# Kernel tuning notes

Measured on AMD Instinct MI355X. Metric: run time of the kernel, lower is better.

## Reference

```python
import jax, jax.numpy as jnp
import numpy as np

B, L, E, H = 4, 2048, 1024, 16
D = E // H  # per-head dim

def setup_inputs() -> dict:
    key = jax.random.key(0)
    ks = jax.random.split(key, 12)
    xav = lambda k, shape: jax.random.normal(k, shape, jnp.float32) * (2.0 / (shape[0] + shape[-1])) ** 0.5
    embeddings = jax.random.normal(ks[0], (B, L, E), jnp.float32)
    pre_proj_w = xav(ks[1], (E, E)); pre_proj_b = jnp.zeros((E,), jnp.float32)
    pre_sparse_w = xav(ks[2], (E, E)); pre_sparse_b = jnp.zeros((E,), jnp.float32)
    toeplitz_psfs = xav(ks[3], (H, 2 * L - 1, D))
    post_conv_w = xav(ks[4], (E, E)); post_conv_b = jnp.zeros((E,), jnp.float32)
    dens = 0.01
    num_nz = int(L * L * dens)
    idxs = jax.random.randint(ks[5], (num_nz, 2), 0, L)
    vals = jnp.abs(jax.random.normal(ks[6], (num_nz,), jnp.float32))
    sparse = jnp.zeros((L, L), jnp.float32).at[idxs[:, 0], idxs[:, 1]].add(vals)
    ln_gamma = jnp.ones((E,), jnp.float32); ln_beta = jnp.zeros((E,), jnp.float32)
    return {"embeddings": embeddings, "pre_proj_w": pre_proj_w, "pre_proj_b": pre_proj_b,
            "pre_sparse_w": pre_sparse_w, "pre_sparse_b": pre_sparse_b,
            "toeplitz_psfs": toeplitz_psfs, "post_conv_w": post_conv_w, "post_conv_b": post_conv_b,
            "sparse": sparse, "ln_gamma": ln_gamma, "ln_beta": ln_beta}

def reference(embeddings, pre_proj_w, pre_proj_b, pre_sparse_w, pre_sparse_b,
              toeplitz_psfs, post_conv_w, post_conv_b, sparse, ln_gamma, ln_beta):
    b, l, e = embeddings.shape
    h, two_l_m1, d = toeplitz_psfs.shape
    # causal PSF mask: first l taps kept, trailing l-1 zeroed (before softmax)
    psf_mask = jnp.concatenate([jnp.ones((l,)), jnp.zeros((l - 1,))])[None, :, None]
    psfs = jax.nn.softmax(toeplitz_psfs * psf_mask, axis=1)  # softmax over 2l-1 taps
    # pre-projection
    pre = jnp.einsum('ble,oe->blo', embeddings, pre_proj_w) + pre_proj_b
    # pad seq to 2l-1 and split heads: [b, h, 2l-1, d]
    padded = jnp.pad(pre, ((0, 0), (0, l - 1), (0, 0)))
    padded = padded.reshape(b, two_l_m1, h, d).transpose(0, 2, 1, 3)
    # 2D FFT convolution over (seq, per-head-dim)
    psf_fft = jnp.fft.fftn(psfs, axes=(1, 2))              # [h, 2l-1, d]
    emb_fft = jnp.fft.fftn(padded, axes=(2, 3))            # [b, h, 2l-1, d]
    conv = jnp.real(jnp.fft.ifftn(psf_fft[None] * emb_fft, axes=(2, 3)))[:, :, :l, :]
    conv = jax.nn.gelu(conv, approximate=False)
    conv = conv.transpose(0, 2, 1, 3).reshape(b, l, e)
    conv_emb = jnp.einsum('ble,oe->blo', conv, post_conv_w) + post_conv_b
    # sparse branch (causal lower-triangular mask)
    sparse_masked = sparse * jnp.tril(jnp.ones((l, l), sparse.dtype))
    pre_sparse = jnp.einsum('ble,oe->blo', pre, pre_sparse_w) + pre_sparse_b
    sparse_emb = jnp.einsum('ls,bse->ble', sparse_masked, pre_sparse)
    # residual + layernorm (dropout = identity at eval)
    x = conv_emb + sparse_emb + embeddings
    mu = jnp.mean(x, axis=-1, keepdims=True)
    var = jnp.mean(jnp.square(x - mu), axis=-1, keepdims=True)
    return (x - mu) * jax.lax.rsqrt(var + 1e-12) * ln_gamma + ln_beta
```

## Files before the change

kernel.cpp:

```cpp
#include <hip/hip_runtime.h>
#include <hip/hip_bf16.h>
#include <hip/hip_fp16.h>
#include <math.h>

#define B_ 4
#define L_ 2048
#define E_ 1024
#define H_ 16
#define D_ 64
#define NFFT 4096
#define CAP 128

typedef __hip_bfloat16 bf16;
typedef __attribute__((ext_vector_type(8))) short bf16x8;
typedef __attribute__((ext_vector_type(4))) float f32x4;
typedef __attribute__((ext_vector_type(2))) __fp16 f16x2;

typedef __attribute__((address_space(1))) const unsigned int gas_u32;
typedef __attribute__((address_space(3))) unsigned int las_u32;

__device__ __forceinline__ void gload_lds16(const void* g, void* l) {
    __builtin_amdgcn_global_load_lds((gas_u32*)g, (las_u32*)l, 16, 0, 0);
}

#define SL(i) ((i) + ((i) >> 4))
#define LDSN (NFFT + NFFT / 16)
#define FST 65

__device__ __forceinline__ float bfu2f(unsigned short u) {
    return __uint_as_float(((unsigned)u) << 16);
}
__device__ __forceinline__ f16x2 pk2(float a, float b) {
    return __builtin_amdgcn_cvt_pkrtz(a, b);
}

__device__ __forceinline__ int drev64(int k) {
    return ((k & 3) << 4) | (k & 12) | ((k >> 4) & 3);
}

#define C1R 0.923879532511287f
#define C1I -0.382683432365090f
#define C2R 0.707106781186548f
#define C2I -0.707106781186548f
#define C3R 0.382683432365090f
#define C3I -0.923879532511287f

__device__ __forceinline__ void r4dif_w(float& x0r, float& x0i, float& x1r, float& x1i,
                                        float& x2r, float& x2i, float& x3r, float& x3i,
                                        float w1r, float w1i) {
    float a0r = x0r + x2r, a0i = x0i + x2i, a1r = x0r - x2r, a1i = x0i - x2i;
    float a2r = x1r + x3r, a2i = x1i + x3i, a3r = x1r - x3r, a3i = x1i - x3i;
    float y0r = a0r + a2r, y0i = a0i + a2i, y2r = a0r - a2r, y2i = a0i - a2i;
    float y1r = a1r + a3i, y1i = a1i - a3r, y3r = a1r - a3i, y3i = a1i + a3r;
    float w2r = w1r * w1r - w1i * w1i, w2i = 2.0f * w1r * w1i;
    float w3r = w2r * w1r - w2i * w1i, w3i = w2r * w1i + w2i * w1r;
    x0r = y0r; x0i = y0i;
    x1r = y1r * w1r - y1i * w1i; x1i = y1r * w1i + y1i * w1r;
    x2r = y2r * w2r - y2i * w2i; x2i = y2r * w2i + y2i * w2r;
    x3r = y3r * w3r - y3i * w3i; x3i = y3r * w3i + y3i * w3r;
}
__device__ __forceinline__ void r4dif_nt(float& x0r, float& x0i, float& x1r, float& x1i,
                                         float& x2r, float& x2i, float& x3r, float& x3i) {
    float a0r = x0r + x2r, a0i = x0i + x2i, a1r = x0r - x2r, a1i = x0i - x2i;
    float a2r = x1r + x3r, a2i = x1i + x3i, a3r = x1r - x3r, a3i = x1i - x3i;
    x0r = a0r + a2r; x0i = a0i + a2i;
    x2r = a0r - a2r; x2i = a0i - a2i;
    float y1r = a1r + a3i, y1i = a1i - a3r, y3r = a1r - a3i, y3i = a1i + a3r;
    x1r = y1r; x1i = y1i; x3r = y3r; x3i = y3i;
}
__device__ __forceinline__ void r4dit_w(float& x0r, float& x0i, float& x1r, float& x1i,
                                        float& x2r, float& x2i, float& x3r, float& x3i,
                                        float w1r, float w1i) {
    float w2r = w1r * w1r - w1i * w1i, w2i = 2.0f * w1r * w1i;
    float w3r = w2r * w1r - w2i * w1i, w3i = w2r * w1i + w2i * w1r;
    float z1r = x1r * w1r + x1i * w1i, z1i = x1i * w1r - x1r * w1i;
    float z2r = x2r * w2r + x2i * w2i, z2i = x2i * w2r - x2r * w2i;
    float z3r = x3r * w3r + x3i * w3i, z3i = x3i * w3r - x3r * w3i;
    float b0r = x0r + z2r, b0i = x0i + z2i, b1r = x0r - z2r, b1i = x0i - z2i;
    float b2r = z1r + z3r, b2i = z1i + z3i, b3r = z1r - z3r, b3i = z1i - z3i;
    x0r = b0r + b2r; x0i = b0i + b2i;
    x2r = b0r - b2r; x2i = b0i - b2i;
    x1r = b1r - b3i; x1i = b1i + b3r;
    x3r = b1r + b3i; x3i = b1i - b3r;
}
__device__ __forceinline__ void r4dit_nt(float& x0r, float& x0i, float& x1r, float& x1i,
                                         float& x2r, float& x2i, float& x3r, float& x3i) {
    float b0r = x0r + x2r, b0i = x0i + x2i, b1r = x0r - x2r, b1i = x0i - x2i;
    float b2r = x1r + x3r, b2i = x1i + x3i, b3r = x1r - x3r, b3i = x1i - x3i;
    x0r = b0r + b2r; x0i = b0i + b2i;
    x2r = b0r - b2r; x2i = b0i - b2i;
    x1r = b1r - b3i; x1i = b1i + b3r;
    x3r = b1r + b3i; x3i = b1i - b3r;
}

__device__ __forceinline__ void fftA_fwd(float* xr, float* xi, float wpr, float wpi) {
    r4dif_w(xr[0], xi[0], xr[4], xi[4], xr[8], xi[8], xr[12], xi[12], wpr, wpi);
    r4dif_w(xr[1], xi[1], xr[5], xi[5], xr[9], xi[9], xr[13], xi[13],
            wpr * C1R - wpi * C1I, wpr * C1I + wpi * C1R);
    r4dif_w(xr[2], xi[2], xr[6], xi[6], xr[10], xi[10], xr[14], xi[14],
            wpr * C2R - wpi * C2I, wpr * C2I + wpi * C2R);
    r4dif_w(xr[3], xi[3], xr[7], xi[7], xr[11], xi[11], xr[15], xi[15],
            wpr * C3R - wpi * C3I, wpr * C3I + wpi * C3R);
    float s2r = wpr * wpr - wpi * wpi, s2i = 2.0f * wpr * wpi;
    float w4r = s2r * s2r - s2i * s2i, w4i = 2.0f * s2r * s2i;
#pragma unroll
    for (int g = 0; g < 4; ++g)
        r4dif_w(xr[4 * g], xi[4 * g], xr[4 * g + 1], xi[4 * g + 1], xr[4 * g + 2],
                xi[4 * g + 2], xr[4 * g + 3], xi[4 * g + 3], w4r, w4i);
}
__device__ __forceinline__ void fftA_inv(float* xr, float* xi, float wpr, float wpi) {
    float s2r = wpr * wpr - wpi * wpi, s2i = 2.0f * wpr * wpi;
    float w4r = s2r * s2r - s2i * s2i, w4i = 2.0f * s2r * s2i;
#pragma unroll
    for (int g = 0; g < 4; ++g)
        r4dit_w(xr[4 * g], xi[4 * g], xr[4 * g + 1], xi[4 * g + 1], xr[4 * g + 2],
                xi[4 * g + 2], xr[4 * g + 3], xi[4 * g + 3], w4r, w4i);
    r4dit_w(xr[0], xi[0], xr[4], xi[4], xr[8], xi[8], xr[12], xi[12], wpr, wpi);
    r4dit_w(xr[1], xi[1], xr[5], xi[5], xr[9], xi[9], xr[13], xi[13],
            wpr * C1R - wpi * C1I, wpr * C1I + wpi * C1R);
    r4dit_w(xr[2], xi[2], xr[6], xi[6], xr[10], xi[10], xr[14], xi[14],
            wpr * C2R - wpi * C2I, wpr * C2I + wpi * C2R);
    r4dit_w(xr[3], xi[3], xr[7], xi[7], xr[11], xi[11], xr[15], xi[15],
            wpr * C3R - wpi * C3I, wpr * C3I + wpi * C3R);
}
__device__ __forceinline__ void fftB_fwd(float* xr, float* xi, float wor, float woi) {
    r4dif_w(xr[0], xi[0], xr[4], xi[4], xr[8], xi[8], xr[12], xi[12], wor, woi);
    r4dif_w(xr[1], xi[1], xr[5], xi[5], xr[9], xi[9], xr[13], xi[13],
            wor * C1R - woi * C1I, wor * C1I + woi * C1R);
    r4dif_w(xr[2], xi[2], xr[6], xi[6], xr[10], xi[10], xr[14], xi[14],
            wor * C2R - woi * C2I, wor * C2I + woi * C2R);
    r4dif_w(xr[3], xi[3], xr[7], xi[7], xr[11], xi[11], xr[15], xi[15],
            wor * C3R - woi * C3I, wor * C3I + woi * C3R);
    float s2r = wor * wor - woi * woi, s2i = 2.0f * wor * woi;
    float w4r = s2r * s2r - s2i * s2i, w4i = 2.0f * s2r * s2i;
#pragma unroll
    for (int g = 0; g < 4; ++g)
        r4dif_w(xr[4 * g], xi[4 * g], xr[4 * g + 1], xi[4 * g + 1], xr[4 * g + 2],
                xi[4 * g + 2], xr[4 * g + 3], xi[4 * g + 3], w4r, w4i);
}
__device__ __forceinline__ void fftB_inv(float* xr, float* xi, float wor, float woi) {
    float s2r = wor * wor - woi * woi, s2i = 2.0f * wor * woi;
    float w4r = s2r * s2r - s2i * s2i, w4i = 2.0f * s2r * s2i;
#pragma unroll
    for (int g = 0; g < 4; ++g)
        r4dit_w(xr[4 * g], xi[4 * g], xr[4 * g + 1], xi[4 * g + 1], xr[4 * g + 2],
                xi[4 * g + 2], xr[4 * g + 3], xi[4 * g + 3], w4r, w4i);
    r4dit_w(xr[0], xi[0], xr[4], xi[4], xr[8], xi[8], xr[12], xi[12], wor, woi);
    r4dit_w(xr[1], xi[1], xr[5], xi[5], xr[9], xi[9], xr[13], xi[13],
            wor * C1R - woi * C1I, wor * C1I + woi * C1R);
    r4dit_w(xr[2], xi[2], xr[6], xi[6], xr[10], xi[10], xr[14], xi[14],
            wor * C2R - woi * C2I, wor * C2I + woi * C2R);
    r4dit_w(xr[3], xi[3], xr[7], xi[7], xr[11], xi[11], xr[15], xi[15],
            wor * C3R - woi * C3I, wor * C3I + woi * C3R);
}
__device__ __forceinline__ void fftC_fwd(float* xr, float* xi) {
    r4dif_w(xr[0], xi[0], xr[4], xi[4], xr[8], xi[8], xr[12], xi[12], 1.0f, 0.0f);
    r4dif_w(xr[1], xi[1], xr[5], xi[5], xr[9], xi[9], xr[13], xi[13], C1R, C1I);
    r4dif_w(xr[2], xi[2], xr[6], xi[6], xr[10], xi[10], xr[14], xi[14], C2R, C2I);
    r4dif_w(xr[3], xi[3], xr[7], xi[7], xr[11], xi[11], xr[15], xi[15], C3R, C3I);
#pragma unroll
    for (int g = 0; g < 4; ++g)
        r4dif_nt(xr[4 * g], xi[4 * g], xr[4 * g + 1], xi[4 * g + 1], xr[4 * g + 2],
                 xi[4 * g + 2], xr[4 * g + 3], xi[4 * g + 3]);
}
__device__ __forceinline__ void fftC_inv(float* xr, float* xi) {
#pragma unroll
    for (int g = 0; g < 4; ++g)
        r4dit_nt(xr[4 * g], xi[4 * g], xr[4 * g + 1], xi[4 * g + 1], xr[4 * g + 2],
                 xi[4 * g + 2], xr[4 * g + 3], xi[4 * g + 3]);
    r4dit_w(xr[0], xi[0], xr[4], xi[4], xr[8], xi[8], xr[12], xi[12], 1.0f, 0.0f);
    r4dit_w(xr[1], xi[1], xr[5], xi[5], xr[9], xi[9], xr[13], xi[13], C1R, C1I);
    r4dit_w(xr[2], xi[2], xr[6], xi[6], xr[10], xi[10], xr[14], xi[14], C2R, C2I);
    r4dit_w(xr[3], xi[3], xr[7], xi[7], xr[11], xi[11], xr[15], xi[15], C3R, C3I);
}

template <int CONJ, int STRIDE>
__device__ inline void fft64h(f16x2* __restrict__ X, int tid,
                              const float2* __restrict__ tw) {
    for (int st = 0; st < 3; ++st) {
        int q = 1 << (4 - 2 * st);
        __syncthreads();
        for (int it = 0; it < 4; ++it) {
            int w = tid + (it << 8);
            int lc = w & 63, bc = w >> 6;
            int p = bc & (q - 1);
            int basev = ((bc & ~(q - 1)) << 2) | p;
            int i0 = basev * STRIDE + lc, i1 = i0 + q * STRIDE,
                i2 = i1 + q * STRIDE, i3 = i2 + q * STRIDE;
            f16x2 h0 = X[i0], h1 = X[i1], h2 = X[i2], h3 = X[i3];
            float x0r = (float)h0.x, x0i = (float)h0.y;
            float x1r = (float)h1.x, x1i = (float)h1.y;
            float x2r = (float)h2.x, x2i = (float)h2.y;
            float x3r = (float)h3.x, x3i = (float)h3.y;
            float a0r = x0r + x2r, a0i = x0i + x2i;
            float a1r = x0r - x2r, a1i = x0i - x2i;
            float a2r = x1r + x3r, a2i = x1i + x3i;
            float a3r = x1r - x3r, a3i = x1i - x3i;
            float y0r = a0r + a2r, y0i = a0i + a2i;
            float y2r = a0r - a2r, y2i = a0i - a2i;
            float y1r, y1i, y3r, y3i;
            if (!CONJ) {
                y1r = a1r + a3i; y1i = a1i - a3r;
                y3r = a1r - a3i; y3i = a1i + a3r;
            } else {
                y1r = a1r - a3i; y1i = a1i + a3r;
                y3r = a1r + a3i; y3i = a1i - a3r;
            }
            int e = (p << (2 * st)) * 64;
            float2 w1 = tw[e];
            float w1x = w1.x, w1y = CONJ ? -w1.y : w1.y;
            float w2x = w1x * w1x - w1y * w1y, w2y = 2.0f * w1x * w1y;
            float w3x = w2x * w1x - w2y * w1y, w3y = w2x * w1y + w2y * w1x;
            X[i0] = pk2(y0r, y0i);
            X[i1] = pk2(y1r * w1x - y1i * w1y, y1r * w1y + y1i * w1x);
            X[i2] = pk2(y2r * w2x - y2i * w2y, y2r * w2y + y2i * w2x);
            X[i3] = pk2(y3r * w3x - y3i * w3y, y3r * w3y + y3i * w3x);
        }
    }
    __syncthreads();
}

#define NB_TW 16
#define NB_CVT 8192
#define NB_CVTW 3072
#define NB_TF 512
#define NB_SP 2048
__global__ __launch_bounds__(256) void k_prologue(const float* __restrict__ emb,
                                                  const float* __restrict__ W1,
                                                  const float* __restrict__ W2,
                                                  const float* __restrict__ W3,
                                                  const float* __restrict__ psfs,
                                                  const float* __restrict__ Sp,
                                                  float2* __restrict__ tw,
                                                  bf16* __restrict__ embb,
                                                  bf16* __restrict__ Wb,
                                                  float* __restrict__ psfT,
                                                  int* __restrict__ nnz,
                                                  int* __restrict__ idxs,
                                                  float* __restrict__ vals) {
    __shared__ float tile[64][65];
    __shared__ int cnt;
    int tid = threadIdx.x;
    int blk = blockIdx.x;
    if (blk < NB_TW) {
        int k = blk * 256 + tid;
        float ang = -(float)k * (float)(M_PI / 2048.0);
        tw[k] = make_float2(cosf(ang), sinf(ang));
        return;
    }
    blk -= NB_TW;
    if (blk < NB_CVT) {
        int i = (blk * 256 + tid) * 4;
        float4 v = *(const float4*)(emb + i);
        bf16 tmp[4];
        tmp[0] = __float2bfloat16(v.x); tmp[1] = __float2bfloat16(v.y);
        tmp[2] = __float2bfloat16(v.z); tmp[3] = __float2bfloat16(v.w);
        *(ushort4*)(embb + i) = *(ushort4*)tmp;
        return;
    }
    blk -= NB_CVT;
    if (blk < NB_CVTW) {
        int w = blk >> 10;
        const float* src = (w == 0) ? W1 : (w == 1) ? W2 : W3;
        int i = ((blk & 1023) * 256 + tid) * 4;
        float4 v = *(const float4*)(src + i);
        bf16 tmp[4];
        tmp[0] = __float2bfloat16(v.x); tmp[1] = __float2bfloat16(v.y);
        tmp[2] = __float2bfloat16(v.z); tmp[3] = __float2bfloat16(v.w);
        *(ushort4*)(Wb + (size_t)w * E_ * E_ + i) = *(ushort4*)tmp;
        return;
    }
    blk -= NB_CVTW;
    if (blk < NB_TF) {
        int z = blk >> 5;
        int r0 = (blk & 31) * 64;
        const float* in = psfs + (size_t)z * (2 * L_ - 1) * D_;
        float* out = psfT + (size_t)z * D_ * L_;
        int tx4 = (tid & 15) * 4, ty = tid >> 4;
#pragma unroll
        for (int k = 0; k < 4; ++k) {
            int r = ty + 16 * k;
            float4 v = *(const float4*)&in[(size_t)(r0 + r) * D_ + tx4];
            tile[r][tx4 + 0] = v.x; tile[r][tx4 + 1] = v.y;
            tile[r][tx4 + 2] = v.z; tile[r][tx4 + 3] = v.w;
        }
        __syncthreads();
#pragma unroll
        for (int k = 0; k < 4; ++k) {
            int c = ty + 16 * k;
            float4 w;
            w.x = tile[tx4 + 0][c]; w.y = tile[tx4 + 1][c];
            w.z = tile[tx4 + 2][c]; w.w = tile[tx4 + 3][c];
            *(float4*)&out[(size_t)c * L_ + r0 + tx4] = w;
        }
        return;
    }
    blk -= NB_TF;
    {
        int l = blk;
        if (tid == 0) cnt = 0;
        __syncthreads();
        const float* row = Sp + (size_t)l * L_;
        for (int s = tid; s <= l; s += 256) {
            float v = row[s];
            if (v != 0.0f) {
                int slot = atomicAdd(&cnt, 1);
                if (slot < CAP) { idxs[l * CAP + slot] = s; vals[l * CAP + slot] = v; }
            }
        }
        __syncthreads();
        if (tid == 0) nnz[l] = min(cnt, CAP);
    }
}

__device__ __forceinline__ void gemm_body(void* smemraw, int flat, int nwgx,
                                          const bf16* __restrict__ A,
                                          const bf16* __restrict__ Wt,
                                          const float* __restrict__ bias,
                                          bf16* __restrict__ Cb,
                                          int nwg, int N, int K) {
    bf16* As = (bf16*)smemraw;
    bf16* Bs = As + 64 * 64;
    int tid = threadIdx.x;
    int lane = tid & 63, w = tid >> 6;
    int wr = w >> 1, wc = w & 1;

    int cpx = nwg >> 3;
    int swz = (flat & 7) * cpx + (flat >> 3);
    int bx = (swz % nwgx) * 128;
    int by = (swz / nwgx) * 64;

    f32x4 zz = {0.0f, 0.0f, 0.0f, 0.0f};
    f32x4 acc[2][4];
#pragma unroll
    for (int m = 0; m < 2; ++m)
#pragma unroll
        for (int n = 0; n < 4; ++n) acc[m][n] = zz;

    int koff = (lane >> 4) * 8;
    int rsub = lane & 15;

    for (int k0 = 0; k0 < K; k0 += 64) {
#pragma unroll
        for (int i = 0; i < 2; ++i) {
            int c = tid + i * 256;
            int row = c >> 3;
            int kb = (c & 7) * 8;
            int kbs = kb ^ ((row & 7) << 3);
            gload_lds16(A + (size_t)(by + row) * K + k0 + kbs, &As[c * 8]);
        }
#pragma unroll
        for (int i = 0; i < 4; ++i) {
            int c = tid + i * 256;
            int row = c >> 3;
            int kb = (c & 7) * 8;
            int kbs = kb ^ ((row & 7) << 3);
            gload_lds16(Wt + (size_t)(bx + row) * K + k0 + kbs, &Bs[c * 8]);
        }
        __syncthreads();
#pragma unroll
        for (int half = 0; half < 2; ++half) {
            int ko = koff + half * 32;
            bf16x8 af[2], bfv[4];
#pragma unroll
            for (int m = 0; m < 2; ++m) {
                int R = wr * 32 + m * 16 + rsub;
                af[m] = *(const bf16x8*)&As[R * 64 + (ko ^ ((R & 7) << 3))];
            }
#pragma unroll
            for (int n = 0; n < 4; ++n) {
                int R = wc * 64 + n * 16 + rsub;
                bfv[n] = *(const bf16x8*)&Bs[R * 64 + (ko ^ ((R & 7) << 3))];
            }
#pragma unroll
            for (int m = 0; m < 2; ++m)
#pragma unroll
                for (int n = 0; n < 4; ++n)
                    acc[m][n] = __builtin_amdgcn_mfma_f32_16x16x32_bf16(af[m], bfv[n], acc[m][n], 0, 0, 0);
        }
        __syncthreads();
    }

    int cq = (lane >> 4) * 4;
    int cr = lane & 15;
#pragma unroll
    for (int m = 0; m < 2; ++m) {
        int row0 = by + wr * 32 + m * 16 + cq;
#pragma unroll
        for (int n = 0; n < 4; ++n) {
            int col = bx + wc * 64 + n * 16 + cr;
            float bv = bias[col];
#pragma unroll
            for (int j = 0; j < 4; ++j) {
                float v = acc[m][n][j] + bv;
                Cb[(size_t)(row0 + j) * N + col] = __float2bfloat16(v);
            }
        }
    }
}

__device__ __forceinline__ void khat_body(void* smemraw, int blk,
                                          const float* __restrict__ psfT,
                                          f16x2* __restrict__ Khat,
                                          const float2* __restrict__ tw) {
    f16x2* fl = (f16x2*)smemraw;
    float* red = (float*)(fl + LDSN);
    int u = blk & 63, h = blk >> 6;
    int tid = threadIdx.x;
    const float* col = psfT + ((size_t)(h * D_ + u)) * L_;
    int p = tid;

    float2 twp = tw[p];
    float2 two = tw[(tid & 15) * 16];

    float v[8];
#pragma unroll
    for (int j = 0; j < 8; ++j) v[j] = col[p + 256 * j];

    float lm = v[0];
#pragma unroll
    for (int j = 1; j < 8; ++j) lm = fmaxf(lm, v[j]);
    red[tid] = lm; __syncthreads();
    for (int off = 128; off > 0; off >>= 1) {
        if (tid < off) red[tid] = fmaxf(red[tid], red[tid + off]);
        __syncthreads();
    }
    float M = fmaxf(red[0], 0.0f);
    __syncthreads();

    float e[8];
    float ls = 0.0f;
#pragma unroll
    for (int j = 0; j < 8; ++j) { e[j] = expf(v[j] - M); ls += e[j]; }
    red[tid] = ls; __syncthreads();
    for (int off = 128; off > 0; off >>= 1) {
        if (tid < off) red[tid] += red[tid + off];
        __syncthreads();
    }
    float Z = red[0] + (float)(L_ - 1) * expf(-M);
    float invZ = 1.0f / Z;
    float cval = expf(-M) * invZ;

    float xr[16], xi[16];
#pragma unroll
    for (int j = 0; j < 16; ++j) {
        int i = p + 256 * j;
        xr[j] = (j < 8) ? e[j] * invZ : ((i == 2048) ? 0.0f : cval);
        xi[j] = 0.0f;
    }
    __syncthreads();

    fftA_fwd(xr, xi, twp.x, twp.y);
#pragma unroll
    for (int j = 0; j < 16; ++j) fl[SL(p + 256 * j)] = pk2(xr[j], xi[j]);
    __syncthreads();
    {
        int bb = tid >> 4, o = tid & 15;
#pragma unroll
        for (int j = 0; j < 16; ++j) {
            f16x2 hh = fl[SL(bb * 256 + o + 16 * j)];
            xr[j] = (float)hh.x; xi[j] = (float)hh.y;
        }
        fftB_fwd(xr, xi, two.x, two.y);
#pragma unroll
        for (int j = 0; j < 16; ++j)
            fl[SL(bb * 256 + o + 16 * j)] = pk2(xr[j], xi[j]);
    }
    __syncthreads();
#pragma unroll
    for (int j = 0; j < 16; ++j) {
        f16x2 hh = fl[SL(16 * tid + j)];
        xr[j] = (float)hh.x; xi[j] = (float)hh.y;
    }
    fftC_fwd(xr, xi);

    float sc = 1.0f / (float)NFFT;
    f16x2* outp = Khat + ((size_t)h * D_ + u) * NFFT + 16 * tid;
#pragma unroll
    for (int j = 0; j < 16; ++j) outp[j] = pk2(xr[j] * sc, xi[j] * sc);
}

__device__ __forceinline__ void dfft_body(void* smemraw, int blk,
                                          f16x2* __restrict__ Khat,
                                          const float2* __restrict__ tw) {
    f16x2* X = (f16x2*)smemraw;
    int tid = threadIdx.x;
    int f0 = (blk & 63) * 64, h = blk >> 6;
    f16x2* kb = Khat + (size_t)h * D_ * NFFT;
    for (int i = tid; i < 4096; i += 256) {
        int uu = i >> 6, fc = i & 63;
        X[i] = kb[(size_t)uu * NFFT + f0 + fc];
    }
    fft64h<0, 64>(X, tid, tw);
    float sc = 1.0f / 64.0f;
    for (int i = tid; i < 4096; i += 256) {
        int s = i >> 6, fc = i & 63;
        f16x2 v = X[i];
        kb[(size_t)drev64(s) * NFFT + f0 + fc] = pk2((float)v.x * sc, (float)v.y * sc);
    }
}

__device__ __forceinline__ void vfft_body(void* smemraw, int blk,
                                          const bf16* __restrict__ preb,
                                          f16x2* __restrict__ Xv,
                                          const float2* __restrict__ tw) {
    f16x2* X = (f16x2*)smemraw;
    int tid = threadIdx.x;
    int l0 = (blk & 31) * 64, h = (blk >> 5) & 15, b = blk >> 9;
    const bf16* src = preb + ((size_t)(b * L_ + l0)) * E_ + h * 64;
#pragma unroll
    for (int it = 0; it < 2; ++it) {
        int c = tid + it * 256;
        int lc = c >> 3, v8 = (c & 7) * 8;
        bf16x8 xv8 = *(const bf16x8*)(src + (size_t)lc * E_ + v8);
#pragma unroll
        for (int j = 0; j < 8; ++j)
            X[(v8 + j) * FST + lc] = pk2(bfu2f((unsigned short)xv8[j]), 0.0f);
    }
    fft64h<0, FST>(X, tid, tw);
    for (int i = tid; i < 33 * 64; i += 256) {
        int k = i >> 6, lc = i & 63;
        Xv[((size_t)(b * H_ + h) * 33 + k) * L_ + l0 + lc] = X[drev64(k) * FST + lc];
    }
}

__global__ __launch_bounds__(256) void k_gemm1_khat(const bf16* __restrict__ A,
                                                    const bf16* __restrict__ Wt,
                                                    const float* __restrict__ bias,
                                                    bf16* __restrict__ Cb,
                                                    const float* __restrict__ psfT,
                                                    f16x2* __restrict__ Khat,
                                                    const float2* __restrict__ tw) {
    __shared__ __align__(16) char smem[24576];
    int blk = blockIdx.x;
    if (blk < 1024)
        gemm_body(smem, blk, 8, A, Wt, bias, Cb, 1024, E_, E_);
    else
        khat_body(smem, blk - 1024, psfT, Khat, tw);
}

__global__ __launch_bounds__(256) void k_gemm2_dfft_vfft(const bf16* __restrict__ A,
                                                         const bf16* __restrict__ Wt,
                                                         const float* __restrict__ bias,
                                                         bf16* __restrict__ Cb,
                                                         f16x2* __restrict__ Khat,
                                                         f16x2* __restrict__ Xv,
                                                         const float2* __restrict__ tw) {
    __shared__ __align__(16) char smem[24576];
    int blk = blockIdx.x;
    if (blk < 1024)
        gemm_body(smem, blk, 8, A, Wt, bias, Cb, 1024, E_, E_);
    else if (blk < 2048)
        dfft_body(smem, blk - 1024, Khat, tw);
    else
        vfft_body(smem, blk - 2048, A, Xv, tw);
}

__global__ __launch_bounds__(256) void k_gemm3(const bf16* __restrict__ A,
                                               const bf16* __restrict__ Wt,
                                               const float* __restrict__ bias,
                                               bf16* __restrict__ Cb) {
    __shared__ __align__(16) char smem[24576];
    gemm_body(smem, blockIdx.x, 8, A, Wt, bias, Cb, 1024, E_, E_);
}

__global__ __launch_bounds__(256) void k_seqconv(f16x2* __restrict__ Xv,
                                                 const f16x2* __restrict__ Khat,
                                                 const float2* __restrict__ tw) {
    __shared__ f16x2 fl[LDSN];
    int k = blockIdx.x, h = blockIdx.y, b = blockIdx.z;
    int tid = threadIdx.x, p = tid;
    f16x2* col = Xv + ((size_t)(b * H_ + h) * 33 + k) * L_;

    float2 twp = tw[p];
    float2 two = tw[(tid & 15) * 16];

    float xr[16], xi[16];
#pragma unroll
    for (int j = 0; j < 16; ++j) {
        if (j < 8) {
            f16x2 z = col[p + 256 * j];
            xr[j] = (float)z.x; xi[j] = (float)z.y;
        } else { xr[j] = 0.0f; xi[j] = 0.0f; }
    }
    fftA_fwd(xr, xi, twp.x, twp.y);
#pragma unroll
    for (int j = 0; j < 16; ++j) fl[SL(p + 256 * j)] = pk2(xr[j], xi[j]);
    __syncthreads();
    {
        int bb = tid >> 4, o = tid & 15;
#pragma unroll
        for (int j = 0; j < 16; ++j) {
            f16x2 hh = fl[SL(bb * 256 + o + 16 * j)];
            xr[j] = (float)hh.x; xi[j] = (float)hh.y;
        }
        fftB_fwd(xr, xi, two.x, two.y);
#pragma unroll
        for (int j = 0; j < 16; ++j)
            fl[SL(bb * 256 + o + 16 * j)] = pk2(xr[j], xi[j]);
    }
    __syncthreads();
    {
        const f16x2* khp = Khat + ((size_t)h * 64 + k) * NFFT + 16 * tid;
        f16x2 kk[16];
#pragma unroll
        for (int j = 0; j < 16; ++j) kk[j] = khp[j];
#pragma unroll
        for (int j = 0; j < 16; ++j) {
            f16x2 hh = fl[SL(16 * tid + j)];
            xr[j] = (float)hh.x; xi[j] = (float)hh.y;
        }
        fftC_fwd(xr, xi);
#pragma unroll
        for (int j = 0; j < 16; ++j) {
            float kr = (float)kk[j].x, ki = (float)kk[j].y;
            float ar = xr[j], ai = xi[j];
            xr[j] = ar * kr - ai * ki;
            xi[j] = ar * ki + ai * kr;
        }
        fftC_inv(xr, xi);
#pragma unroll
        for (int j = 0; j < 16; ++j) fl[SL(16 * tid + j)] = pk2(xr[j], xi[j]);
    }
    __syncthreads();
    {
        int bb = tid >> 4, o = tid & 15;
#pragma unroll
        for (int j = 0; j < 16; ++j) {
            f16x2 hh = fl[SL(bb * 256 + o + 16 * j)];
            xr[j] = (float)hh.x; xi[j] = (float)hh.y;
        }
        fftB_inv(xr, xi, two.x, two.y);
#pragma unroll
        for (int j = 0; j < 16; ++j)
            fl[SL(bb * 256 + o + 16 * j)] = pk2(xr[j], xi[j]);
    }
    __syncthreads();
#pragma unroll
    for (int j = 0; j < 16; ++j) {
        f16x2 hh = fl[SL(p + 256 * j)];
        xr[j] = (float)hh.x; xi[j] = (float)hh.y;
    }
    fftA_inv(xr, xi, twp.x, twp.y);
#pragma unroll
    for (int j = 0; j < 8; ++j)
        col[p + 256 * j] = pk2(xr[j], xi[j]);
}

__global__ __launch_bounds__(256) void k_vifft(const f16x2* __restrict__ Xv,
                                               bf16* __restrict__ actb,
                                               const float2* __restrict__ tw) {
    __shared__ f16x2 X[64 * FST];
    int l0 = blockIdx.x * 64, h = blockIdx.y, b = blockIdx.z;
    int tid = threadIdx.x;
    for (int i = tid; i < 33 * 64; i += 256) {
        int k = i >> 6, lc = i & 63;
        X[k * FST + lc] = Xv[((size_t)(b * H_ + h) * 33 + k) * L_ + l0 + lc];
    }
    __syncthreads();
    for (int i = tid; i < 31 * 64; i += 256) {
        int k = 33 + (i >> 6), lc = i & 63;
        f16x2 z = X[(64 - k) * FST + lc];
        X[k * FST + lc] = pk2((float)z.x, -(float)z.y);
    }
    fft64h<1, FST>(X, tid, tw);
    bf16* dst = actb + ((size_t)(b * L_ + l0)) * E_ + h * 64;
#pragma unroll
    for (int it = 0; it < 2; ++it) {
        int c = tid + it * 256;
        int lc = c >> 3, m8 = (c & 7) * 8;
        unsigned short o[8];
#pragma unroll
        for (int j = 0; j < 8; ++j) {
            float x = (float)X[drev64(m8 + j) * FST + lc].x;
            float g = 0.5f * x * (1.0f + erff(x * 0.70710678118654752f));
            bf16 bb = __float2bfloat16(g);
            o[j] = *(unsigned short*)&bb;
        }
        *(ushort4*)(dst + (size_t)lc * E_ + m8)     = make_ushort4(o[0], o[1], o[2], o[3]);
        *(ushort4*)(dst + (size_t)lc * E_ + m8 + 4) = make_ushort4(o[4], o[5], o[6], o[7]);
    }
}

__global__ __launch_bounds__(256) void k_spmm_ln(const int* __restrict__ nnz,
                                                 const int* __restrict__ idxs,
                                                 const float* __restrict__ vals,
                                                 const bf16* __restrict__ P,
                                                 const bf16* __restrict__ accbb,
                                                 const float* __restrict__ emb,
                                                 const float* __restrict__ gamma,
                                                 const float* __restrict__ beta,
                                                 float* __restrict__ outp) {
    __shared__ int sidx[CAP];
    __shared__ float sval[CAP];
    __shared__ float red[256];
    int l = blockIdx.x, b = blockIdx.y, tid = threadIdx.x;
    int n = nnz[l];
    for (int j = tid; j < n; j += 256) {
        sidx[j] = idxs[l * CAP + j];
        sval[j] = vals[l * CAP + j];
    }
    __syncthreads();
    size_t off = (size_t)tid * 4;
    size_t rowbase = ((size_t)(b * L_ + l)) * E_;
    ushort4 a4 = *(const ushort4*)(accbb + rowbase + off);
    float4 e4 = *(const float4*)(emb + rowbase + off);
    float x0 = bfu2f(a4.x) + e4.x;
    float x1 = bfu2f(a4.y) + e4.y;
    float x2 = bfu2f(a4.z) + e4.z;
    float x3 = bfu2f(a4.w) + e4.w;
    const bf16* Pb = P + (size_t)b * L_ * E_;
    for (int j = 0; j < n; ++j) {
        float v = sval[j];
        ushort4 p = *(const ushort4*)(Pb + (size_t)sidx[j] * E_ + off);
        x0 += v * bfu2f(p.x); x1 += v * bfu2f(p.y);
        x2 += v * bfu2f(p.z); x3 += v * bfu2f(p.w);
    }
    red[tid] = x0 + x1 + x2 + x3; __syncthreads();
    for (int o2 = 128; o2 > 0; o2 >>= 1) {
        if (tid < o2) red[tid] += red[tid + o2];
        __syncthreads();
    }
    float mu = red[0] * (1.0f / E_);
    __syncthreads();
    float d0 = x0 - mu, d1 = x1 - mu, d2 = x2 - mu, d3 = x3 - mu;
    red[tid] = d0 * d0 + d1 * d1 + d2 * d2 + d3 * d3; __syncthreads();
    for (int o2 = 128; o2 > 0; o2 >>= 1) {
        if (tid < o2) red[tid] += red[tid + o2];
        __syncthreads();
    }
    float inv = rsqrtf(red[0] * (1.0f / E_) + 1e-12f);
    float4 g4 = *(const float4*)(gamma + off);
    float4 b4 = *(const float4*)(beta + off);
    float4 o4;
    o4.x = d0 * inv * g4.x + b4.x;
    o4.y = d1 * inv * g4.y + b4.y;
    o4.z = d2 * inv * g4.z + b4.z;
    o4.w = d3 * inv * g4.w + b4.w;
    *(float4*)(outp + rowbase + off) = o4;
}

extern "C" void kernel_launch(void* const* d_in, const int* in_sizes, int n_in,
                              void* d_out, int out_size, void* d_ws, size_t ws_size,
                              hipStream_t stream) {
    const float* emb    = (const float*)d_in[0];
    const float* W1     = (const float*)d_in[1];
    const float* b1     = (const float*)d_in[2];
    const float* W2     = (const float*)d_in[3];
    const float* b2     = (const float*)d_in[4];
    const float* psfs   = (const float*)d_in[5];
    const float* W3     = (const float*)d_in[6];
    const float* b3     = (const float*)d_in[7];
    const float* sparse = (const float*)d_in[8];
    const float* gamma  = (const float*)d_in[9];
    const float* beta   = (const float*)d_in[10];
    float* outp = (float*)d_out;

    const size_t BLE  = (size_t)B_ * L_ * E_;
    const size_t EE   = (size_t)E_ * E_;
    const size_t KSZ  = (size_t)H_ * D_ * NFFT;
    const size_t XVSZ = (size_t)B_ * H_ * 33 * L_;

    bf16*   accbb      = (bf16*)d_ws;
    bf16*   pre_sparse = accbb + BLE;
    f16x2*  Khat       = (f16x2*)(pre_sparse + BLE);
    f16x2*  Xv         = Khat + KSZ;
    bf16*   preb       = (bf16*)(Xv + XVSZ);
    bf16*   actb       = preb + BLE;
    bf16*   W1b        = actb + BLE;
    bf16*   W2b        = W1b + EE;
    bf16*   W3b        = W2b + EE;
    float2* twd        = (float2*)(W3b + EE);
    int*    s_nnz      = (int*)(twd + NFFT);
    int*    s_idx      = s_nnz + L_;
    float*  s_val      = (float*)(s_idx + (size_t)L_ * CAP);
    float*  psfT       = (float*)Xv;

    k_prologue<<<NB_TW + NB_CVT + NB_CVTW + NB_TF + NB_SP, 256, 0, stream>>>(
        emb, W1, W2, W3, psfs, sparse, twd, actb, W1b, psfT, s_nnz, s_idx, s_val);

    k_gemm1_khat<<<2048, 256, 0, stream>>>(actb, W1b, b1, preb, psfT, Khat, twd);

    k_gemm2_dfft_vfft<<<4096, 256, 0, stream>>>(preb, W2b, b2, pre_sparse, Khat, Xv, twd);

    k_seqconv<<<dim3(33, H_, B_), 256, 0, stream>>>(Xv, Khat, twd);

    k_vifft<<<dim3(L_ / 64, H_, B_), 256, 0, stream>>>(Xv, actb, twd);

    k_gemm3<<<1024, 256, 0, stream>>>(actb, W3b, b3, accbb);

    k_spmm_ln<<<dim3(L_, B_), 256, 0, stream>>>(
        s_nnz, s_idx, s_val, pre_sparse, accbb, emb, gamma, beta, outp);
}
```

Measured before the change: 195.4 us.

## Move sparse-branch GEMM to co-run with inverse FFT instead of forward FFTs

The pre_sparse GEMM blocks move out of the kernel they shared with the forward FFTs (dfft/vfft) and into a new combined kernel that also runs the inverse FFT with GELU. The forward FFTs now run alone in a kernel with a smaller shared-memory footprint, and the standalone vifft kernel is removed. The aim is to rebalance the cross-stage schedule so that the GEMM overlaps the vifft stage and the seqconv stage can start earlier. Block counts and per-kernel occupancy change as a result.

```diff
diff --git a/kernel.cpp b/kernel.cpp
--- a/kernel.cpp
+++ b/kernel.cpp
@@ -524,6 +524,42 @@
     }
 }
 
+__device__ __forceinline__ void vifft_body(void* smemraw, int blk,
+                                           const f16x2* __restrict__ Xv,
+                                           bf16* __restrict__ actb,
+                                           const float2* __restrict__ tw) {
+    f16x2* X = (f16x2*)smemraw;
+    int tid = threadIdx.x;
+    int l0 = (blk & 31) * 64, h = (blk >> 5) & 15, b = blk >> 9;
+    for (int i = tid; i < 33 * 64; i += 256) {
+        int k = i >> 6, lc = i & 63;
+        X[k * FST + lc] = Xv[((size_t)(b * H_ + h) * 33 + k) * L_ + l0 + lc];
+    }
+    __syncthreads();
+    for (int i = tid; i < 31 * 64; i += 256) {
+        int k = 33 + (i >> 6), lc = i & 63;
+        f16x2 z = X[(64 - k) * FST + lc];
+        X[k * FST + lc] = pk2((float)z.x, -(float)z.y);
+    }
+    fft64h<1, FST>(X, tid, tw);
+    bf16* dst = actb + ((size_t)(b * L_ + l0)) * E_ + h * 64;
+#pragma unroll
+    for (int it = 0; it < 2; ++it) {
+        int c = tid + it * 256;
+        int lc = c >> 3, m8 = (c & 7) * 8;
+        unsigned short o[8];
+#pragma unroll
+        for (int j = 0; j < 8; ++j) {
+            float x = (float)X[drev64(m8 + j) * FST + lc].x;
+            float g = 0.5f * x * (1.0f + erff(x * 0.70710678118654752f));
+            bf16 bb = __float2bfloat16(g);
+            o[j] = *(unsigned short*)&bb;
+        }
+        *(ushort4*)(dst + (size_t)lc * E_ + m8)     = make_ushort4(o[0], o[1], o[2], o[3]);
+        *(ushort4*)(dst + (size_t)lc * E_ + m8 + 4) = make_ushort4(o[4], o[5], o[6], o[7]);
+    }
+}
+
 __global__ __launch_bounds__(256) void k_gemm1_khat(const bf16* __restrict__ A,
                                                     const bf16* __restrict__ Wt,
                                                     const float* __restrict__ bias,
@@ -539,21 +575,31 @@
         khat_body(smem, blk - 1024, psfT, Khat, tw);
 }
 
-__global__ __launch_bounds__(256) void k_gemm2_dfft_vfft(const bf16* __restrict__ A,
-                                                         const bf16* __restrict__ Wt,
-                                                         const float* __restrict__ bias,
-                                                         bf16* __restrict__ Cb,
-                                                         f16x2* __restrict__ Khat,
-                                                         f16x2* __restrict__ Xv,
-                                                         const float2* __restrict__ tw) {
+__global__ __launch_bounds__(256) void k_dfft_vfft(f16x2* __restrict__ Khat,
+                                                   const bf16* __restrict__ preb,
+                                                   f16x2* __restrict__ Xv,
+                                                   const float2* __restrict__ tw) {
+    __shared__ __align__(16) char smem[16640];
+    int blk = blockIdx.x;
+    if (blk < 1024)
+        dfft_body(smem, blk, Khat, tw);
+    else
+        vfft_body(smem, blk - 1024, preb, Xv, tw);
+}
+
+__global__ __launch_bounds__(256) void k_vifft_gemm2(const bf16* __restrict__ A,
+                                                     const bf16* __restrict__ Wt,
+                                                     const float* __restrict__ bias,
+                                                     bf16* __restrict__ Cb,
+                                                     const f16x2* __restrict__ Xv,
+                                                     bf16* __restrict__ actb,
+                                                     const float2* __restrict__ tw) {
     __shared__ __align__(16) char smem[24576];
     int blk = blockIdx.x;
     if (blk < 1024)
         gemm_body(smem, blk, 8, A, Wt, bias, Cb, 1024, E_, E_);
-    else if (blk < 2048)
-        dfft_body(smem, blk - 1024, Khat, tw);
     else
-        vfft_body(smem, blk - 2048, A, Xv, tw);
+        vifft_body(smem, blk - 1024, Xv, actb, tw);
 }
 
 __global__ __launch_bounds__(256) void k_gemm3(const bf16* __restrict__ A,
@@ -645,41 +691,6 @@
 #pragma unroll
     for (int j = 0; j < 8; ++j)
         col[p + 256 * j] = pk2(xr[j], xi[j]);
-}
-
-__global__ __launch_bounds__(256) void k_vifft(const f16x2* __restrict__ Xv,
-                                               bf16* __restrict__ actb,
-                                               const float2* __restrict__ tw) {
-    __shared__ f16x2 X[64 * FST];
-    int l0 = blockIdx.x * 64, h = blockIdx.y, b = blockIdx.z;
-    int tid = threadIdx.x;
-    for (int i = tid; i < 33 * 64; i += 256) {
-        int k = i >> 6, lc = i & 63;
-        X[k * FST + lc] = Xv[((size_t)(b * H_ + h) * 33 + k) * L_ + l0 + lc];
-    }
-    __syncthreads();
-    for (int i = tid; i < 31 * 64; i += 256) {
-        int k = 33 + (i >> 6), lc = i & 63;
-        f16x2 z = X[(64 - k) * FST + lc];
-        X[k * FST + lc] = pk2((float)z.x, -(float)z.y);
-    }
-    fft64h<1, FST>(X, tid, tw);
-    bf16* dst = actb + ((size_t)(b * L_ + l0)) * E_ + h * 64;
-#pragma unroll
-    for (int it = 0; it < 2; ++it) {
-        int c = tid + it * 256;
-        int lc = c >> 3, m8 = (c & 7) * 8;
-        unsigned short o[8];
-#pragma unroll
-        for (int j = 0; j < 8; ++j) {
-            float x = (float)X[drev64(m8 + j) * FST + lc].x;
-            float g = 0.5f * x * (1.0f + erff(x * 0.70710678118654752f));
-            bf16 bb = __float2bfloat16(g);
-            o[j] = *(unsigned short*)&bb;
-        }
-        *(ushort4*)(dst + (size_t)lc * E_ + m8)     = make_ushort4(o[0], o[1], o[2], o[3]);
-        *(ushort4*)(dst + (size_t)lc * E_ + m8 + 4) = make_ushort4(o[4], o[5], o[6], o[7]);
-    }
 }
 
 __global__ __launch_bounds__(256) void k_spmm_ln(const int* __restrict__ nnz,
@@ -781,11 +792,11 @@
 
     k_gemm1_khat<<<2048, 256, 0, stream>>>(actb, W1b, b1, preb, psfT, Khat, twd);
 
-    k_gemm2_dfft_vfft<<<4096, 256, 0, stream>>>(preb, W2b, b2, pre_sparse, Khat, Xv, twd);
+    k_dfft_vfft<<<3072, 256, 0, stream>>>(Khat, preb, Xv, twd);
 
     k_seqconv<<<dim3(33, H_, B_), 256, 0, stream>>>(Xv, Khat, twd);
 
-    k_vifft<<<dim3(L_ / 64, H_, B_), 256, 0, stream>>>(Xv, actb, twd);
+    k_vifft_gemm2<<<3072, 256, 0, stream>>>(preb, W2b, b2, pre_sparse, Xv, actb, twd);
 
     k_gemm3<<<1024, 256, 0, stream>>>(actb, W3b, b3, accbb);
 
```

Result: no change. 197.2 us (+0.9%).
